# Kernel tuning notes

Measured on AMD Instinct MI355X. Metric: run time of the kernel, lower is better.

Reference implementation:

```python
import jax, jax.numpy as jnp
import numpy as np

B, Cin, H, W = 4, 256, 96, 96
CC = 64      # corr_channels
K = 5        # corr_kernel_size
OC = 32      # out_channels
PAD = K // 2 # pad='k' with odd K -> symmetric pad 2


def setup_inputs() -> dict:
    key = jax.random.key(0)
    k0, k1, k2, k3, k4 = jax.random.split(key, 5)
    x = jax.random.normal(k0, (B, Cin, H, W), jnp.float32)
    extract_w = jax.random.normal(k1, (CC, Cin, 3, 3), jnp.float32) * 0.02
    extract_b = jax.random.normal(k2, (CC,), jnp.float32) * 0.02
    reg_w = jax.random.normal(k3, (OC, CC, K, K), jnp.float32) * 0.02
    reg_b = jax.random.normal(k4, (OC,), jnp.float32) * 0.02
    return {"x": x, "extract_w": extract_w, "extract_b": extract_b,
            "reg_w": reg_w, "reg_b": reg_b}


def reference(x, extract_w, extract_b, reg_w, reg_b):
    # extract_input: 3x3 conv, padding 1 (NCHW / OIHW)
    f = jax.lax.conv_general_dilated(
        x, extract_w, window_strides=(1, 1), padding=[(1, 1), (1, 1)],
        dimension_numbers=("NCHW", "OIHW", "NCHW"))
    f = f + extract_b[None, :, None, None]  # [B, CC, H, W]

    # LocalAutoCorr2D: per-channel product of each center feature with its
    # KxK neighborhood (pad='k', stride=1 -> corr grid == feature grid).
    xp = jnp.pad(f, ((0, 0), (0, 0), (PAD, PAD), (PAD, PAD)))
    nh, nw = H, W
    # patches[b,c,u,v,i,j] = xp[b,c,i+u,j+v]; static KxK loop, vectorized over B/C/HW
    patches = jnp.stack(
        [jnp.stack([xp[:, :, u:u + nh, v:v + nw] for v in range(K)], axis=2)
         for u in range(K)], axis=2)               # [B, CC, K, K, nh, nw]
    center = patches[:, :, K // 2, K // 2]         # [B, CC, nh, nw]
    corr = patches * center[:, :, None, None]      # [B, CC, K, K, nh, nw]

    # full contraction over (c,u,v) for every corr-grid location.
    y = jnp.einsum("bcuvij,ocuv->boij", corr, reg_w) + reg_b[None, :, None, None]
    # permute=True -> [B, OC, nh, nw]
    return y
```

## Files before the change

### kernel.cpp

```cpp
#include <hip/hip_runtime.h>
#include <hip/hip_bf16.h>

#define BATCH 4
#define CIN 256
#define H 96
#define W 96
#define CC 64
#define OC 32

typedef __attribute__((ext_vector_type(8))) short bf16x8;
typedef __attribute__((ext_vector_type(4))) float f32x4;
typedef __attribute__((ext_vector_type(4))) unsigned short u16x4;
typedef __attribute__((ext_vector_type(4))) unsigned int u32x4;

#define XT_OFF  0
#define WT_OFF  19668992
#define RWT_OFF 19963904
#define FT_OFF  20066304

__device__ inline unsigned short f2bf(float v) {
    __hip_bfloat16 t = __float2bfloat16(v);
    return *reinterpret_cast<unsigned short*>(&t);
}
__device__ inline float bf2f(short b) {
    return __uint_as_float(((unsigned int)(unsigned short)b) << 16);
}

__device__ inline void gload_lds16(const __hip_bfloat16* g, void* l) {
    __builtin_amdgcn_global_load_lds(
        (const __attribute__((address_space(1))) unsigned int*)g,
        (__attribute__((address_space(3))) unsigned int*)l, 16, 0, 0);
}

__global__ __launch_bounds__(256) void prep_kernel(
    const float* __restrict__ ew, const float* __restrict__ rw,
    __hip_bfloat16* __restrict__ wt, __hip_bfloat16* __restrict__ rwt,
    __hip_bfloat16* __restrict__ ft)
{
    const int bid = blockIdx.x;
    const int tid = threadIdx.x;
    if (bid < 576) {
        int idx = bid * 256 + tid;
        if (idx >= 9 * 4 * 32 * 16 * 8) return;
        int e   = idx & 7;
        int m   = (idx >> 3) & 15;
        int cb  = (idx >> 7) & 31;
        int ccg = (idx >> 12) & 3;
        int k   = idx >> 14;
        int cc = ccg * 16 + m, ci = cb * 8 + e;
        wt[idx] = __float2bfloat16(ew[(cc * CIN + ci) * 9 + k]);
    } else if (bid < 776) {
        int idx = (bid - 576) * 256 + tid;
        if (idx >= 50 * 2 * 64 * 8) return;
        int e    = idx & 7;
        int lane = (idx >> 3) & 63;
        int mt   = (idx >> 9) & 1;
        int kc   = idx >> 10;
        int g = lane >> 4, m = lane & 15;
        int o  = mt * 16 + m;
        int k  = kc * 32 + g * 8 + e;
        int uv = k >> 6, c = k & 63;
        rwt[idx] = __float2bfloat16(rw[(o * CC + c) * 25 + uv]);
    } else {
        int idx = (bid - 776) * 256 + tid;
        if (idx >= 4 * 6272) return;
        int b = idx / 6272, t = idx % 6272;
        int q = t & 7, pid = t >> 3;
        int r, c;
        if (pid < 400) {
            int rr = pid / 100;
            r = (rr < 2) ? rr : rr + 96;
            c = pid % 100;
        } else {
            int p2 = pid - 400;
            r = 2 + (p2 >> 2);
            int c2 = p2 & 3;
            c = (c2 < 2) ? c2 : c2 + 96;
        }
        *(u32x4*)(ft + ((size_t)((b * 100 + r) * 100 + c)) * 64 + q * 8) = (u32x4){0u,0u,0u,0u};
    }
}

__global__ __launch_bounds__(256) void xt_kernel(const float* __restrict__ x,
                                                 __hip_bfloat16* __restrict__ xt)
{
    const int r = blockIdx.x;
    const int b = blockIdx.y;
    const int tid = threadIdx.x;
    __hip_bfloat16* rowp = xt + ((size_t)(b * 98 + r)) * 98 * 256;
    const int gi = r - 1;

    if (gi < 0 || gi >= H) {
        unsigned int* p = (unsigned int*)rowp;
        for (int t = tid; t < 98 * 256 / 2; t += 256) p[t] = 0u;
        return;
    }

    __shared__ __hip_bfloat16 lds[96][258];

    for (int cich = 0; cich < 8; ++cich) {
        int ci = cich * 32 + (tid >> 3);
        const float* src = x + ((size_t)((b * CIN + ci) * H + gi)) * W;
        for (int coli = 0; coli < 3; ++coli) {
            int col = coli * 32 + (tid & 7) * 4;
            float4 v = *(const float4*)(src + col);
            lds[col + 0][ci] = __float2bfloat16(v.x);
            lds[col + 1][ci] = __float2bfloat16(v.y);
            lds[col + 2][ci] = __float2bfloat16(v.z);
            lds[col + 3][ci] = __float2bfloat16(v.w);
        }
    }
    __syncthreads();

    unsigned int* dst = (unsigned int*)rowp;
    for (int it = 0; it < 48; ++it) {
        int col = it * 2 + (tid >> 7);
        int ci2 = tid & 127;
        unsigned int v = *(unsigned int*)&lds[col][ci2 * 2];
        dst[(col + 1) * 128 + ci2] = v;
    }
    if (tid < 128) dst[tid] = 0u;
    else           dst[97 * 128 + (tid - 128)] = 0u;
}

__global__ __launch_bounds__(128) void conv_mfma3_kernel(
    const __hip_bfloat16* __restrict__ xt, const __hip_bfloat16* __restrict__ wt,
    const float* __restrict__ eb, __hip_bfloat16* __restrict__ ft)
{
    const int jb = blockIdx.x;
    const int iy = blockIdx.y;
    const int zz = blockIdx.z;
    const int b = zz >> 1, ch = zz & 1;
    const int j0 = jb * 32, i0 = iy * 2;
    const int tid = threadIdx.x;
    const int wid = tid >> 6;
    const int lane = tid & 63;
    const int g = lane >> 4, m = lane & 15;

    __shared__ __align__(16) char bbuf[2][9216];

    const int nslot = 5 - wid;
    const __hip_bfloat16* src0; const __hip_bfloat16* src1;
    const __hip_bfloat16* src2; const __hip_bfloat16* src3;
    const __hip_bfloat16* src4;
    int dst0, dst1, dst2, dst3, dst4;
    {
        const int base = wid * 320;
#define SLOT_INIT(J, SRC, DST)                                                  \
        {                                                                       \
            int U = base + (J) * 64 + lane;                                     \
            if (U > 575) U = 575;                                               \
            int s = U & 3, pxr = U >> 2;                                        \
            int px = pxr % 36, r = pxr / 36;                                    \
            int q = s ^ ((px >> 1) & 3);                                        \
            SRC = xt + ((size_t)((b * 98 + i0 + r) * 98 + j0 + px)) * 256 + q * 8; \
            DST = (base + (J) * 64) * 16;                                       \
        }
        SLOT_INIT(0, src0, dst0)
        SLOT_INIT(1, src1, dst1)
        SLOT_INIT(2, src2, dst2)
        SLOT_INIT(3, src3, dst3)
        SLOT_INIT(4, src4, dst4)
#undef SLOT_INIT
    }

#define STAGE(T, NB)                                                            \
    {                                                                           \
        const int co = (T) * 32;                                                \
        char* lb = &bbuf[(NB)][0];                                              \
        gload_lds16(src0 + co, lb + dst0);                                      \
        gload_lds16(src1 + co, lb + dst1);                                      \
        gload_lds16(src2 + co, lb + dst2);                                      \
        gload_lds16(src3 + co, lb + dst3);                                      \
        if (nslot > 4) gload_lds16(src4 + co, lb + dst4);                       \
    }

    STAGE(0, 0)
    __syncthreads();

    f32x4 acc00 = (f32x4){0.f,0.f,0.f,0.f}, acc01 = (f32x4){0.f,0.f,0.f,0.f};
    f32x4 acc10 = (f32x4){0.f,0.f,0.f,0.f}, acc11 = (f32x4){0.f,0.f,0.f,0.f};

    const __hip_bfloat16* wA = wt + (ch * 2) * 4096 + g * 128 + m * 8;

    for (int t = 0; t < 8; ++t) {
        if (t < 7) STAGE(t + 1, (t + 1) & 1)

        const char* bb = &bbuf[t & 1][0];
        const __hip_bfloat16* wa = wA + t * 512;
#pragma unroll
        for (int ku = 0; ku < 3; ++ku) {
#pragma unroll
            for (int kv = 0; kv < 3; ++kv) {
                const int k = ku * 3 + kv;
                bf16x8 a0 = *(const bf16x8*)(wa + k * 16384);
                bf16x8 a1 = *(const bf16x8*)(wa + k * 16384 + 4096);
                const int r = wid + ku;
                const int px0 = m + kv, px1 = px0 + 16;
                bf16x8 b0 = *(const bf16x8*)(bb + ((r * 36 + px0) * 4 + (g ^ ((px0 >> 1) & 3))) * 16);
                bf16x8 b1 = *(const bf16x8*)(bb + ((r * 36 + px1) * 4 + (g ^ ((px1 >> 1) & 3))) * 16);
                acc00 = __builtin_amdgcn_mfma_f32_16x16x32_bf16(a0, b0, acc00, 0, 0, 0);
                acc01 = __builtin_amdgcn_mfma_f32_16x16x32_bf16(a0, b1, acc01, 0, 0, 0);
                acc10 = __builtin_amdgcn_mfma_f32_16x16x32_bf16(a1, b0, acc10, 0, 0, 0);
                acc11 = __builtin_amdgcn_mfma_f32_16x16x32_bf16(a1, b1, acc11, 0, 0, 0);
            }
        }
        __syncthreads();
    }
#undef STAGE

    __hip_bfloat16* out = ft + ((size_t)((b * 100 + i0 + wid + 2) * 100 + (j0 + 2))) * 64;
#pragma unroll
    for (int mt = 0; mt < 2; ++mt) {
        const int ccb = (ch * 2 + mt) * 16 + g * 4;
        float bias[4];
#pragma unroll
        for (int r = 0; r < 4; ++r) bias[r] = eb[ccb + r];
        f32x4 aN0 = (mt == 0) ? acc00 : acc10;
        f32x4 aN1 = (mt == 0) ? acc01 : acc11;
        u16x4 p0, p1;
#pragma unroll
        for (int r = 0; r < 4; ++r) {
            p0[r] = f2bf(aN0[r] + bias[r]);
            p1[r] = f2bf(aN1[r] + bias[r]);
        }
        *(u16x4*)(out + (0 * 16 + m) * 64 + ccb) = p0;
        *(u16x4*)(out + (1 * 16 + m) * 64 + ccb) = p1;
    }
}

__global__ __launch_bounds__(256) void corrproj_mfma2_kernel(
    const __hip_bfloat16* __restrict__ ft, const __hip_bfloat16* __restrict__ rwt,
    const float* __restrict__ rb, float* __restrict__ y)
{
    const int jb = blockIdx.x;
    const int iy = blockIdx.y;
    const int b  = blockIdx.z;
    const int jc0 = jb * 32, i0 = iy * 2;
    const int tid = threadIdx.x;
    const int wave = tid >> 6, lane = tid & 63;
    const int g = lane >> 4, m = lane & 15;
    const int rw = wave >> 1, pw = wave & 1;

    __shared__ __align__(16) char wnd[6 * 36 * 128];
    __shared__ __align__(16) char asub[2][5 * 2 * 1024];

    {
        const __hip_bfloat16* base = ft + ((size_t)((b * 100 + i0) * 100 + jc0)) * 64;
#pragma unroll
        for (int it = 0; it < 7; ++it) {
            int u = it * 256 + tid;
            if (u < 1728) {
                int q = u & 7, rc = u >> 3;
                int col = rc % 36, r = rc / 36;
                u32x4 v = *(const u32x4*)(base + ((size_t)(r * 100 + col)) * 64 + q * 8);
                *(u32x4*)(wnd + (r * 36 + col) * 128 + ((q ^ (col & 7)) << 4)) = v;
            }
        }
    }
    {
        const u32x4* src = (const u32x4*)rwt;
        u32x4* dst = (u32x4*)&asub[0][0];
        dst[tid] = src[tid];
        dst[tid + 256] = src[tid + 256];
        if (tid < 128) dst[tid + 512] = src[tid + 512];
    }
    __syncthreads();

    float cen[16];
    {
        const int colc = pw * 16 + m + 2;
        const char* cb = wnd + ((rw + 2) * 36 + colc) * 128;
        bf16x8 c0 = *(const bf16x8*)(cb + ((g ^ (colc & 7)) << 4));
        bf16x8 c1 = *(const bf16x8*)(cb + (((4 + g) ^ (colc & 7)) << 4));
#pragma unroll
        for (int e = 0; e < 8; ++e) {
            cen[e]     = bf2f(c0[e]);
            cen[8 + e] = bf2f(c1[e]);
        }
    }

    f32x4 acc0 = (f32x4){0.f, 0.f, 0.f, 0.f};
    f32x4 acc1 = (f32x4){0.f, 0.f, 0.f, 0.f};

    for (int sc = 0; sc < 10; ++sc) {
        u32x4 p0, p1, p2;
        const bool pf = (sc < 9);
        if (pf) {
            const u32x4* src = (const u32x4*)rwt + (sc + 1) * 640;
            p0 = src[tid];
            p1 = src[tid + 256];
            if (tid < 128) p2 = src[tid + 512];
        }

        const char* ab = &asub[sc & 1][0];
#pragma unroll
        for (int kk = 0; kk < 5; ++kk) {
            const int kc = sc * 5 + kk;
            const int uv = kc >> 1, h = kc & 1;
            const int u = uv / 5, v = uv - u * 5;
            bf16x8 a0 = *(const bf16x8*)(ab + (kk * 2 + 0) * 1024 + lane * 16);
            bf16x8 a1 = *(const bf16x8*)(ab + (kk * 2 + 1) * 1024 + lane * 16);
            const int col = pw * 16 + m + v;
            const char* sb = wnd + ((rw + u) * 36 + col) * 128;
            bf16x8 s = *(const bf16x8*)(sb + (((h * 4 + g) ^ (col & 7)) << 4));
            bf16x8 hb;
#pragma unroll
            for (int e = 0; e < 8; ++e)
                hb[e] = (short)f2bf(bf2f(s[e]) * cen[h * 8 + e]);
            acc0 = __builtin_amdgcn_mfma_f32_16x16x32_bf16(a0, hb, acc0, 0, 0, 0);
            acc1 = __builtin_amdgcn_mfma_f32_16x16x32_bf16(a1, hb, acc1, 0, 0, 0);
        }

        if (pf) {
            u32x4* dst = (u32x4*)&asub[(sc + 1) & 1][0];
            dst[tid] = p0;
            dst[tid + 256] = p1;
            if (tid < 128) dst[tid + 512] = p2;
        }
        __syncthreads();
    }

    const int i = i0 + rw, j0 = jc0 + pw * 16;
#pragma unroll
    for (int r = 0; r < 4; ++r) {
        int o0 = g * 4 + r;
        y[((size_t)(b * OC + o0) * H + i) * W + j0 + m] = acc0[r] + rb[o0];
        int o1 = 16 + g * 4 + r;
        y[((size_t)(b * OC + o1) * H + i) * W + j0 + m] = acc1[r] + rb[o1];
    }
}

extern "C" void kernel_launch(void* const* d_in, const int* in_sizes, int n_in,
                              void* d_out, int out_size, void* d_ws, size_t ws_size,
                              hipStream_t stream) {
    const float* x  = (const float*)d_in[0];
    const float* ew = (const float*)d_in[1];
    const float* eb = (const float*)d_in[2];
    const float* rw = (const float*)d_in[3];
    const float* rb = (const float*)d_in[4];
    float* y = (float*)d_out;

    char* ws = (char*)d_ws;
    __hip_bfloat16* xt  = (__hip_bfloat16*)(ws + XT_OFF);
    __hip_bfloat16* wt  = (__hip_bfloat16*)(ws + WT_OFF);
    __hip_bfloat16* rwt = (__hip_bfloat16*)(ws + RWT_OFF);
    __hip_bfloat16* ft  = (__hip_bfloat16*)(ws + FT_OFF);

    prep_kernel<<<874, 256, 0, stream>>>(ew, rw, wt, rwt, ft);
    xt_kernel<<<dim3(98, BATCH), 256, 0, stream>>>(x, xt);
    conv_mfma3_kernel<<<dim3(3, 48, 2 * BATCH), 128, 0, stream>>>(xt, wt, eb, ft);
    corrproj_mfma2_kernel<<<dim3(3, 48, BATCH), 256, 0, stream>>>(ft, rwt, rb, y);
}
```

Measured before the change: 58.96 us.

## Merge prep and transpose kernels, widen conv tiles to four output rows

Folds the weight-prep and input-transpose kernels into one launch, which saves a kernel launch and lets the two kinds of blocks overlap. The transpose writes and the halo zeroing now use 16-byte vector stores, and the LDS tile padding is changed so those accesses stay aligned. The conv kernel now computes four output rows per block with 256 threads, so each 6-row input halo staged in LDS is reused across more rows. The trade-offs are larger LDS use per block and half as many blocks in the conv grid.

```diff
diff --git a/kernel.cpp b/kernel.cpp
--- a/kernel.cpp
+++ b/kernel.cpp
@@ -32,71 +32,72 @@
         (__attribute__((address_space(3))) unsigned int*)l, 16, 0, 0);
 }
 
-__global__ __launch_bounds__(256) void prep_kernel(
-    const float* __restrict__ ew, const float* __restrict__ rw,
+__global__ __launch_bounds__(256) void prep_xt_kernel(
+    const float* __restrict__ x, const float* __restrict__ ew,
+    const float* __restrict__ rw, __hip_bfloat16* __restrict__ xt,
     __hip_bfloat16* __restrict__ wt, __hip_bfloat16* __restrict__ rwt,
     __hip_bfloat16* __restrict__ ft)
 {
     const int bid = blockIdx.x;
     const int tid = threadIdx.x;
-    if (bid < 576) {
-        int idx = bid * 256 + tid;
-        if (idx >= 9 * 4 * 32 * 16 * 8) return;
-        int e   = idx & 7;
-        int m   = (idx >> 3) & 15;
-        int cb  = (idx >> 7) & 31;
-        int ccg = (idx >> 12) & 3;
-        int k   = idx >> 14;
-        int cc = ccg * 16 + m, ci = cb * 8 + e;
-        wt[idx] = __float2bfloat16(ew[(cc * CIN + ci) * 9 + k]);
-    } else if (bid < 776) {
-        int idx = (bid - 576) * 256 + tid;
-        if (idx >= 50 * 2 * 64 * 8) return;
-        int e    = idx & 7;
-        int lane = (idx >> 3) & 63;
-        int mt   = (idx >> 9) & 1;
-        int kc   = idx >> 10;
-        int g = lane >> 4, m = lane & 15;
-        int o  = mt * 16 + m;
-        int k  = kc * 32 + g * 8 + e;
-        int uv = k >> 6, c = k & 63;
-        rwt[idx] = __float2bfloat16(rw[(o * CC + c) * 25 + uv]);
-    } else {
-        int idx = (bid - 776) * 256 + tid;
-        if (idx >= 4 * 6272) return;
-        int b = idx / 6272, t = idx % 6272;
-        int q = t & 7, pid = t >> 3;
-        int r, c;
-        if (pid < 400) {
-            int rr = pid / 100;
-            r = (rr < 2) ? rr : rr + 96;
-            c = pid % 100;
+
+    if (bid >= 392) {
+        const int pb = bid - 392;
+        if (pb < 576) {
+            int idx = pb * 256 + tid;
+            int e   = idx & 7;
+            int m   = (idx >> 3) & 15;
+            int cb  = (idx >> 7) & 31;
+            int ccg = (idx >> 12) & 3;
+            int k   = idx >> 14;
+            int cc = ccg * 16 + m, ci = cb * 8 + e;
+            wt[idx] = __float2bfloat16(ew[(cc * CIN + ci) * 9 + k]);
+        } else if (pb < 776) {
+            int idx = (pb - 576) * 256 + tid;
+            if (idx >= 50 * 2 * 64 * 8) return;
+            int e    = idx & 7;
+            int lane = (idx >> 3) & 63;
+            int mt   = (idx >> 9) & 1;
+            int kc   = idx >> 10;
+            int g = lane >> 4, m = lane & 15;
+            int o  = mt * 16 + m;
+            int k  = kc * 32 + g * 8 + e;
+            int uv = k >> 6, c = k & 63;
+            rwt[idx] = __float2bfloat16(rw[(o * CC + c) * 25 + uv]);
         } else {
-            int p2 = pid - 400;
-            r = 2 + (p2 >> 2);
-            int c2 = p2 & 3;
-            c = (c2 < 2) ? c2 : c2 + 96;
-        }
-        *(u32x4*)(ft + ((size_t)((b * 100 + r) * 100 + c)) * 64 + q * 8) = (u32x4){0u,0u,0u,0u};
-    }
-}
-
-__global__ __launch_bounds__(256) void xt_kernel(const float* __restrict__ x,
-                                                 __hip_bfloat16* __restrict__ xt)
-{
-    const int r = blockIdx.x;
-    const int b = blockIdx.y;
-    const int tid = threadIdx.x;
+            int idx = (pb - 776) * 256 + tid;
+            if (idx >= 4 * 6272) return;
+            int b = idx / 6272, t = idx % 6272;
+            int q = t & 7, pid = t >> 3;
+            int r, c;
+            if (pid < 400) {
+                int rr = pid / 100;
+                r = (rr < 2) ? rr : rr + 96;
+                c = pid % 100;
+            } else {
+                int p2 = pid - 400;
+                r = 2 + (p2 >> 2);
+                int c2 = p2 & 3;
+                c = (c2 < 2) ? c2 : c2 + 96;
+            }
+            *(u32x4*)(ft + ((size_t)((b * 100 + r) * 100 + c)) * 64 + q * 8) = (u32x4){0u,0u,0u,0u};
+        }
+        return;
+    }
+
+    const int r = bid % 98;
+    const int b = bid / 98;
     __hip_bfloat16* rowp = xt + ((size_t)(b * 98 + r)) * 98 * 256;
     const int gi = r - 1;
 
     if (gi < 0 || gi >= H) {
-        unsigned int* p = (unsigned int*)rowp;
-        for (int t = tid; t < 98 * 256 / 2; t += 256) p[t] = 0u;
+        u32x4* p = (u32x4*)rowp;
+        const u32x4 z = (u32x4){0u,0u,0u,0u};
+        for (int t = tid; t < 98 * 256 * 2 / 16; t += 256) p[t] = z;
         return;
     }
 
-    __shared__ __hip_bfloat16 lds[96][258];
+    __shared__ __align__(16) __hip_bfloat16 lds[96][264];
 
     for (int cich = 0; cich < 8; ++cich) {
         int ci = cich * 32 + (tid >> 3);
@@ -112,57 +113,55 @@
     }
     __syncthreads();
 
-    unsigned int* dst = (unsigned int*)rowp;
-    for (int it = 0; it < 48; ++it) {
-        int col = it * 2 + (tid >> 7);
-        int ci2 = tid & 127;
-        unsigned int v = *(unsigned int*)&lds[col][ci2 * 2];
-        dst[(col + 1) * 128 + ci2] = v;
-    }
-    if (tid < 128) dst[tid] = 0u;
-    else           dst[97 * 128 + (tid - 128)] = 0u;
-}
-
-__global__ __launch_bounds__(128) void conv_mfma3_kernel(
+    u32x4* dst16 = (u32x4*)rowp;
+#pragma unroll
+    for (int it = 0; it < 12; ++it) {
+        int u = it * 256 + tid;
+        int col = u >> 5, ci8 = u & 31;
+        u32x4 v = *(const u32x4*)&lds[col][ci8 * 8];
+        dst16[(col + 1) * 32 + ci8] = v;
+    }
+    if (tid < 32) dst16[tid] = (u32x4){0u,0u,0u,0u};
+    else if (tid < 64) dst16[97 * 32 + (tid - 32)] = (u32x4){0u,0u,0u,0u};
+}
+
+__global__ __launch_bounds__(256) void conv_mfma4_kernel(
     const __hip_bfloat16* __restrict__ xt, const __hip_bfloat16* __restrict__ wt,
     const float* __restrict__ eb, __hip_bfloat16* __restrict__ ft)
 {
     const int jb = blockIdx.x;
-    const int iy = blockIdx.y;
+    const int iq = blockIdx.y;
     const int zz = blockIdx.z;
     const int b = zz >> 1, ch = zz & 1;
-    const int j0 = jb * 32, i0 = iy * 2;
+    const int j0 = jb * 32, i0 = iq * 4;
     const int tid = threadIdx.x;
     const int wid = tid >> 6;
     const int lane = tid & 63;
     const int g = lane >> 4, m = lane & 15;
 
-    __shared__ __align__(16) char bbuf[2][9216];
-
-    const int nslot = 5 - wid;
+    __shared__ __align__(16) char bbuf[2][14336];
+
+    const int start = (wid < 2) ? wid * 256 : 512 + (wid - 2) * 192;
+    const int nslot = (wid < 2) ? 4 : 3;
+
     const __hip_bfloat16* src0; const __hip_bfloat16* src1;
     const __hip_bfloat16* src2; const __hip_bfloat16* src3;
-    const __hip_bfloat16* src4;
-    int dst0, dst1, dst2, dst3, dst4;
-    {
-        const int base = wid * 320;
+    int dst0, dst1, dst2, dst3;
 #define SLOT_INIT(J, SRC, DST)                                                  \
-        {                                                                       \
-            int U = base + (J) * 64 + lane;                                     \
-            if (U > 575) U = 575;                                               \
-            int s = U & 3, pxr = U >> 2;                                        \
-            int px = pxr % 36, r = pxr / 36;                                    \
-            int q = s ^ ((px >> 1) & 3);                                        \
-            SRC = xt + ((size_t)((b * 98 + i0 + r) * 98 + j0 + px)) * 256 + q * 8; \
-            DST = (base + (J) * 64) * 16;                                       \
-        }
-        SLOT_INIT(0, src0, dst0)
-        SLOT_INIT(1, src1, dst1)
-        SLOT_INIT(2, src2, dst2)
-        SLOT_INIT(3, src3, dst3)
-        SLOT_INIT(4, src4, dst4)
+    {                                                                           \
+        int U = start + (J) * 64 + lane;                                        \
+        if (U > 863) U = 863;                                                   \
+        int s = U & 3, pxr = U >> 2;                                            \
+        int px = pxr % 36, r = pxr / 36;                                        \
+        int q = s ^ ((px >> 1) & 3);                                            \
+        SRC = xt + ((size_t)((b * 98 + i0 + r) * 98 + j0 + px)) * 256 + q * 8;  \
+        DST = (start + (J) * 64) * 16;                                          \
+    }
+    SLOT_INIT(0, src0, dst0)
+    SLOT_INIT(1, src1, dst1)
+    SLOT_INIT(2, src2, dst2)
+    SLOT_INIT(3, src3, dst3)
 #undef SLOT_INIT
-    }
 
 #define STAGE(T, NB)                                                            \
     {                                                                           \
@@ -171,8 +170,7 @@
         gload_lds16(src0 + co, lb + dst0);                                      \
         gload_lds16(src1 + co, lb + dst1);                                      \
         gload_lds16(src2 + co, lb + dst2);                                      \
-        gload_lds16(src3 + co, lb + dst3);                                      \
-        if (nslot > 4) gload_lds16(src4 + co, lb + dst4);                       \
+        if (nslot > 3) gload_lds16(src3 + co, lb + dst3);                       \
     }
 
     STAGE(0, 0)
@@ -347,8 +345,7 @@
     __hip_bfloat16* rwt = (__hip_bfloat16*)(ws + RWT_OFF);
     __hip_bfloat16* ft  = (__hip_bfloat16*)(ws + FT_OFF);
 
-    prep_kernel<<<874, 256, 0, stream>>>(ew, rw, wt, rwt, ft);
-    xt_kernel<<<dim3(98, BATCH), 256, 0, stream>>>(x, xt);
-    conv_mfma3_kernel<<<dim3(3, 48, 2 * BATCH), 128, 0, stream>>>(xt, wt, eb, ft);
+    prep_xt_kernel<<<1266, 256, 0, stream>>>(x, ew, rw, xt, wt, rwt, ft);
+    conv_mfma4_kernel<<<dim3(3, 24, 2 * BATCH), 256, 0, stream>>>(xt, wt, eb, ft);
     corrproj_mfma2_kernel<<<dim3(3, 48, BATCH), 256, 0, stream>>>(ft, rwt, rb, y);
 }
```

Measured after the change: 54.18 us. 8.1% less time.
